# Kernel optimization log

Hardware: AMD Instinct MI355X
Metric: run time of the kernel (lower is better)

The kernel has to match this reference:

```python
import jax, jax.numpy as jnp
import numpy as np

N_QUBITS = 4
N_LAYERS = 6
BATCH = 1 << 20


def _apply_batched_1q(state, U, q):
    # state: [B, 2,2,2,2]; U: [B, 2, 2] per-sample gate on qubit q
    ax = q + 1
    s = jnp.moveaxis(state, ax, -1)
    s = jnp.einsum('bij,b...j->b...i', U, s)
    return jnp.moveaxis(s, -1, ax)


def _apply_shared_1q(state, U, q):
    # U: [2, 2] shared across the batch
    ax = q + 1
    s = jnp.moveaxis(state, ax, -1)
    s = jnp.einsum('ij,...j->...i', U, s)
    return jnp.moveaxis(s, -1, ax)


def _cnot(state, c, t):
    # flip target axis on the control=1 slice
    ca, ta = c + 1, t + 1
    s0 = jax.lax.index_in_dim(state, 0, ca, keepdims=True)
    s1 = jax.lax.index_in_dim(state, 1, ca, keepdims=True)
    return jnp.concatenate([s0, jnp.flip(s1, axis=ta)], axis=ca)


def _circuit(x, weights):
    n = N_QUBITS
    B = x.shape[0]
    # |0...0> state, batched: [B, 2,2,2,2]
    state = jnp.zeros((B,) + (2,) * n, dtype=jnp.complex64)
    state = state.at[(slice(None),) + (0,) * n].set(1.0)
    # Data-encoding RY(x_q) per sample on each wire
    half = x / 2
    c, s = jnp.cos(half), jnp.sin(half)  # [B, n]
    for q in range(n):
        row0 = jnp.stack([c[:, q], -s[:, q]], axis=-1)
        row1 = jnp.stack([s[:, q], c[:, q]], axis=-1)
        U = jnp.stack([row0, row1], axis=-2).astype(jnp.complex64)  # [B,2,2]
        state = _apply_batched_1q(state, U, q)
    # BasicEntanglerLayers: per layer, RX(w) on each wire then CNOT ring
    for l in range(weights.shape[0]):
        for q in range(n):
            t = weights[l, q] / 2
            ct = (jnp.cos(t) + 0j).astype(jnp.complex64)
            st = (-1j * jnp.sin(t)).astype(jnp.complex64)
            U = jnp.stack([jnp.stack([ct, st]), jnp.stack([st, ct])])  # [2,2]
            state = _apply_shared_1q(state, U, q)
        for q in range(n):
            state = _cnot(state, q, (q + 1) % n)
    # <Z_q> from marginal probabilities
    probs = jnp.real(state * jnp.conj(state))  # [B,2,2,2,2] float32
    z = jnp.array([1.0, -1.0], dtype=jnp.float32)
    outs = []
    for q in range(n):
        reduce_axes = tuple(a for a in range(1, n + 1) if a != q + 1)
        outs.append(jnp.tensordot(probs.sum(axis=reduce_axes), z, axes=([1], [0])))
    return jnp.stack(outs, axis=-1)  # [B, n_qubits]


def setup_inputs():
    key = jax.random.key(0)
    k1, k2 = jax.random.split(key)
    x = jax.random.normal(k1, (BATCH, N_QUBITS), dtype=jnp.float32)
    weights = jax.random.normal(k2, (N_LAYERS, N_QUBITS), dtype=jnp.float32) * 0.01
    return {"x": x, "weights": weights}


def reference(x, weights):
    return _circuit(x, weights)
```

## Files before the change

### kernel.cpp

```cpp
#include <hip/hip_runtime.h>
#include <math.h>

#define N_QUBITS 4
#define N_LAYERS 6
#define NW (N_LAYERS * N_QUBITS)

__global__ __launch_bounds__(256) void qprep_kernel(
    const float* __restrict__ weights, float* __restrict__ Ctab)
{
    __shared__ float Wr[16][16];
    __shared__ float Wi[16][16];
    __shared__ float S[4][16][16];
    __shared__ float wc[NW], ws[NW];
    const int tid = threadIdx.x;
    if (tid < NW) {
        float t = weights[tid] * 0.5f;
        wc[tid] = __cosf(t);
        ws[tid] = __sinf(t);
    }
    __syncthreads();

    if (tid < 16) {
        float re[16], im[16];
#pragma unroll
        for (int k = 0; k < 16; ++k) { re[k] = (k == tid) ? 1.f : 0.f; im[k] = 0.f; }
#pragma unroll 1
        for (int l = 0; l < N_LAYERS; ++l) {
#pragma unroll
            for (int q = 0; q < 4; ++q) {
                const float ct = wc[l * 4 + q], sn = ws[l * 4 + q];
                const int mask = 8 >> q;
#pragma unroll
                for (int idx = 0; idx < 16; ++idx) {
                    if (idx & mask) continue;
                    const int j = idx | mask;
                    float r0 = re[idx], u0 = im[idx], r1 = re[j], u1 = im[j];
                    re[idx] = ct * r0 + sn * u1; im[idx] = ct * u0 - sn * r1;
                    re[j]   = ct * r1 + sn * u0; im[j]   = ct * u1 - sn * r0;
                }
            }
#pragma unroll
            for (int q = 0; q < 4; ++q) {
                const int cm = 8 >> q, tm = 8 >> ((q + 1) & 3);
#pragma unroll
                for (int idx = 0; idx < 16; ++idx) {
                    if ((idx & cm) && !(idx & tm)) {
                        const int j = idx | tm;
                        float t0 = re[idx]; re[idx] = re[j]; re[j] = t0;
                        float t1 = im[idx]; im[idx] = im[j]; im[j] = t1;
                    }
                }
            }
        }
#pragma unroll
        for (int k = 0; k < 16; ++k) { Wr[k][tid] = re[k]; Wi[k][tid] = im[k]; }
    }
    __syncthreads();

    {
        const int i = tid >> 4, j = tid & 15;
        float acc0 = 0.f, acc1 = 0.f, acc2 = 0.f, acc3 = 0.f;
#pragma unroll
        for (int k = 0; k < 16; ++k) {
            const float prod = Wr[k][i] * Wr[k][j] + Wi[k][i] * Wi[k][j];
            acc0 += (k & 8) ? -prod : prod;
            acc1 += (k & 4) ? -prod : prod;
            acc2 += (k & 2) ? -prod : prod;
            acc3 += (k & 1) ? -prod : prod;
        }
        S[0][i][j] = acc0; S[1][i][j] = acc1; S[2][i][j] = acc2; S[3][i][j] = acc3;
    }
    __syncthreads();

    if (tid < 81) {
        const int t1 = tid / 27, t2 = (tid / 9) % 3, t3 = (tid / 3) % 3, t4 = tid % 3;
        int zm = 0, xm = 0;
        if (t1 == 1) zm |= 8; else if (t1 == 2) xm |= 8;
        if (t2 == 1) zm |= 4; else if (t2 == 2) xm |= 4;
        if (t3 == 1) zm |= 2; else if (t3 == 2) xm |= 2;
        if (t4 == 1) zm |= 1; else if (t4 == 2) xm |= 1;
#pragma unroll
        for (int q = 0; q < 4; ++q) {
            float acc = 0.f;
#pragma unroll
            for (int i = 0; i < 16; ++i) {
                const float v = S[q][i][i ^ xm];
                acc += (__popc(i & zm) & 1) ? -v : v;
            }
            Ctab[tid * 4 + q] = acc * 0.0625f;
        }
    }
}

__global__ __launch_bounds__(256, 6) void qeval_kernel(
    const float* __restrict__ x, const float* __restrict__ Ctab,
    float* __restrict__ out, int B)
{
    int b = blockIdx.x * 256 + threadIdx.x;
    b = (b < B) ? b : (B - 1);

    const float4 xv = reinterpret_cast<const float4*>(x)[b];
    const float c0 = __cosf(xv.x), s0 = __sinf(xv.x);
    const float c1 = __cosf(xv.y), s1 = __sinf(xv.y);
    const float c2 = __cosf(xv.z), s2 = __sinf(xv.z);
    const float c3 = __cosf(xv.w), s3 = __sinf(xv.w);

    float u9[9], w9[9];
    u9[0] = 1.f;  u9[1] = c1;      u9[2] = s1;
    u9[3] = c0;   u9[4] = c0 * c1; u9[5] = c0 * s1;
    u9[6] = s0;   u9[7] = s0 * c1; u9[8] = s0 * s1;
    w9[0] = 1.f;  w9[1] = c3;      w9[2] = s3;
    w9[3] = c2;   w9[4] = c2 * c3; w9[5] = c2 * s3;
    w9[6] = s2;   w9[7] = s2 * c3; w9[8] = s2 * s3;

    const float4* __restrict__ C4 = reinterpret_cast<const float4*>(Ctab);

    float4 o = make_float4(0.f, 0.f, 0.f, 0.f);
#pragma unroll
    for (int i = 0; i < 9; ++i) {
        float4 t = make_float4(0.f, 0.f, 0.f, 0.f);
#pragma unroll
        for (int j = 0; j < 9; ++j) {
            const float4 c = C4[i * 9 + j];
            const float w = w9[j];
            t.x = fmaf(c.x, w, t.x);
            t.y = fmaf(c.y, w, t.y);
            t.z = fmaf(c.z, w, t.z);
            t.w = fmaf(c.w, w, t.w);
        }
        const float u = u9[i];
        o.x = fmaf(t.x, u, o.x);
        o.y = fmaf(t.y, u, o.y);
        o.z = fmaf(t.z, u, o.z);
        o.w = fmaf(t.w, u, o.w);
    }

    reinterpret_cast<float4*>(out)[b] = o;
}

extern "C" void kernel_launch(void* const* d_in, const int* in_sizes, int n_in,
                              void* d_out, int out_size, void* d_ws, size_t ws_size,
                              hipStream_t stream) {
    const float* x = (const float*)d_in[0];
    const float* weights = (const float*)d_in[1];
    float* out = (float*)d_out;
    float* Ctab = (float*)d_ws;
    const int B = in_sizes[0] / 4;

    qprep_kernel<<<1, 256, 0, stream>>>(weights, Ctab);

    const int grid = (B + 255) / 256;
    qeval_kernel<<<grid, 256, 0, stream>>>(x, Ctab, out, B);
}
```

Measured before the change: 80.61 us.

## Fuse coefficient prep into eval kernel with persistent blocks and readlane broadcast

Merges the table-building and evaluation kernels into one launch of 512 blocks. Each block recomputes the 81x4 coefficient table in shared memory, keeps it in registers and broadcasts entries via readlane, and then processes eight samples per thread in two interleaved streams. This removes a second launch, the global table round-trip and the per-sample table loads, but repeats the serial prep in every block. The grid is hardcoded, so it covers only up to 2^20 samples.

```diff
diff --git a/kernel.cpp b/kernel.cpp
--- a/kernel.cpp
+++ b/kernel.cpp
@@ -1,18 +1,26 @@
 #include <hip/hip_runtime.h>
 #include <math.h>
 
-#define N_QUBITS 4
 #define N_LAYERS 6
-#define NW (N_LAYERS * N_QUBITS)
+#define NW (N_LAYERS * 4)
 
-__global__ __launch_bounds__(256) void qprep_kernel(
-    const float* __restrict__ weights, float* __restrict__ Ctab)
+typedef float vf4 __attribute__((ext_vector_type(4)));
+
+__device__ __forceinline__ float rdl(float v, int lane) {
+    return __int_as_float(__builtin_amdgcn_readlane(__float_as_int(v), lane));
+}
+
+__global__ __launch_bounds__(256, 2) void qfused_kernel(
+    const float* __restrict__ x, const float* __restrict__ weights,
+    float* __restrict__ out, int B)
 {
-    __shared__ float Wr[16][16];
-    __shared__ float Wi[16][16];
-    __shared__ float S[4][16][16];
+    __shared__ float Wr[16][16], Wi[16][16];
+    __shared__ float S4[4][16][16];
     __shared__ float wc[NW], ws[NW];
+    __shared__ vf4 Cs[81];
+
     const int tid = threadIdx.x;
+
     if (tid < NW) {
         float t = weights[tid] * 0.5f;
         wc[tid] = __cosf(t);
@@ -59,16 +67,16 @@
 
     {
         const int i = tid >> 4, j = tid & 15;
-        float acc0 = 0.f, acc1 = 0.f, acc2 = 0.f, acc3 = 0.f;
+        float a0 = 0.f, a1 = 0.f, a2 = 0.f, a3 = 0.f;
 #pragma unroll
         for (int k = 0; k < 16; ++k) {
-            const float prod = Wr[k][i] * Wr[k][j] + Wi[k][i] * Wi[k][j];
-            acc0 += (k & 8) ? -prod : prod;
-            acc1 += (k & 4) ? -prod : prod;
-            acc2 += (k & 2) ? -prod : prod;
-            acc3 += (k & 1) ? -prod : prod;
+            const float p = Wr[k][i] * Wr[k][j] + Wi[k][i] * Wi[k][j];
+            a0 += (k & 8) ? -p : p;
+            a1 += (k & 4) ? -p : p;
+            a2 += (k & 2) ? -p : p;
+            a3 += (k & 1) ? -p : p;
         }
-        S[0][i][j] = acc0; S[1][i][j] = acc1; S[2][i][j] = acc2; S[3][i][j] = acc3;
+        S4[0][i][j] = a0; S4[1][i][j] = a1; S4[2][i][j] = a2; S4[3][i][j] = a3;
     }
     __syncthreads();
 
@@ -79,63 +87,99 @@
         if (t2 == 1) zm |= 4; else if (t2 == 2) xm |= 4;
         if (t3 == 1) zm |= 2; else if (t3 == 2) xm |= 2;
         if (t4 == 1) zm |= 1; else if (t4 == 2) xm |= 1;
+        vf4 c;
 #pragma unroll
         for (int q = 0; q < 4; ++q) {
             float acc = 0.f;
 #pragma unroll
             for (int i = 0; i < 16; ++i) {
-                const float v = S[q][i][i ^ xm];
+                const float v = S4[q][i][i ^ xm];
                 acc += (__popc(i & zm) & 1) ? -v : v;
             }
-            Ctab[tid * 4 + q] = acc * 0.0625f;
+            c[q] = acc * 0.0625f;
         }
+        Cs[tid] = c;
     }
-}
+    __syncthreads();
 
-__global__ __launch_bounds__(256, 6) void qeval_kernel(
-    const float* __restrict__ x, const float* __restrict__ Ctab,
-    float* __restrict__ out, int B)
-{
-    int b = blockIdx.x * 256 + threadIdx.x;
-    b = (b < B) ? b : (B - 1);
+    const int lane = tid & 63;
+    const vf4 Areg = Cs[lane];
+    const vf4 Breg = Cs[64 + (lane < 17 ? lane : 16)];
 
-    const float4 xv = reinterpret_cast<const float4*>(x)[b];
-    const float c0 = __cosf(xv.x), s0 = __sinf(xv.x);
-    const float c1 = __cosf(xv.y), s1 = __sinf(xv.y);
-    const float c2 = __cosf(xv.z), s2 = __sinf(xv.z);
-    const float c3 = __cosf(xv.w), s3 = __sinf(xv.w);
+    const float4* __restrict__ xv4 = reinterpret_cast<const float4*>(x);
+    float4* __restrict__ ov4 = reinterpret_cast<float4*>(out);
+    const int tbase = blockIdx.x * 256 + tid;
+    const int HALF = 512 * 256;
+    const int STRIDE = 2 * HALF;
 
-    float u9[9], w9[9];
-    u9[0] = 1.f;  u9[1] = c1;      u9[2] = s1;
-    u9[3] = c0;   u9[4] = c0 * c1; u9[5] = c0 * s1;
-    u9[6] = s0;   u9[7] = s0 * c1; u9[8] = s0 * s1;
-    w9[0] = 1.f;  w9[1] = c3;      w9[2] = s3;
-    w9[3] = c2;   w9[4] = c2 * c3; w9[5] = c2 * s3;
-    w9[6] = s2;   w9[7] = s2 * c3; w9[8] = s2 * s3;
+#pragma unroll 1
+    for (int k = 0; k < 4; ++k) {
+        int b0 = tbase + k * STRIDE;
+        int b1 = b0 + HALF;
+        b0 = (b0 < B) ? b0 : (B - 1);
+        b1 = (b1 < B) ? b1 : (B - 1);
+        const float4 x0 = xv4[b0];
+        const float4 x1 = xv4[b1];
 
-    const float4* __restrict__ C4 = reinterpret_cast<const float4*>(Ctab);
+        float u9a[9], w9a[9], u9b[9], w9b[9];
+        {
+            const float c0 = __cosf(x0.x), s0 = __sinf(x0.x);
+            const float c1 = __cosf(x0.y), s1 = __sinf(x0.y);
+            const float c2 = __cosf(x0.z), s2 = __sinf(x0.z);
+            const float c3 = __cosf(x0.w), s3 = __sinf(x0.w);
+            u9a[0] = 1.f; u9a[1] = c1;      u9a[2] = s1;
+            u9a[3] = c0;  u9a[4] = c0 * c1; u9a[5] = c0 * s1;
+            u9a[6] = s0;  u9a[7] = s0 * c1; u9a[8] = s0 * s1;
+            w9a[0] = 1.f; w9a[1] = c3;      w9a[2] = s3;
+            w9a[3] = c2;  w9a[4] = c2 * c3; w9a[5] = c2 * s3;
+            w9a[6] = s2;  w9a[7] = s2 * c3; w9a[8] = s2 * s3;
+        }
+        {
+            const float c0 = __cosf(x1.x), s0 = __sinf(x1.x);
+            const float c1 = __cosf(x1.y), s1 = __sinf(x1.y);
+            const float c2 = __cosf(x1.z), s2 = __sinf(x1.z);
+            const float c3 = __cosf(x1.w), s3 = __sinf(x1.w);
+            u9b[0] = 1.f; u9b[1] = c1;      u9b[2] = s1;
+            u9b[3] = c0;  u9b[4] = c0 * c1; u9b[5] = c0 * s1;
+            u9b[6] = s0;  u9b[7] = s0 * c1; u9b[8] = s0 * s1;
+            w9b[0] = 1.f; w9b[1] = c3;      w9b[2] = s3;
+            w9b[3] = c2;  w9b[4] = c2 * c3; w9b[5] = c2 * s3;
+            w9b[6] = s2;  w9b[7] = s2 * c3; w9b[8] = s2 * s3;
+        }
 
-    float4 o = make_float4(0.f, 0.f, 0.f, 0.f);
+        float4 oa = make_float4(0.f, 0.f, 0.f, 0.f);
+        float4 ob = make_float4(0.f, 0.f, 0.f, 0.f);
 #pragma unroll
-    for (int i = 0; i < 9; ++i) {
-        float4 t = make_float4(0.f, 0.f, 0.f, 0.f);
+        for (int i = 0; i < 9; ++i) {
+            float4 ta = make_float4(0.f, 0.f, 0.f, 0.f);
+            float4 tb = make_float4(0.f, 0.f, 0.f, 0.f);
 #pragma unroll
-        for (int j = 0; j < 9; ++j) {
-            const float4 c = C4[i * 9 + j];
-            const float w = w9[j];
-            t.x = fmaf(c.x, w, t.x);
-            t.y = fmaf(c.y, w, t.y);
-            t.z = fmaf(c.z, w, t.z);
-            t.w = fmaf(c.w, w, t.w);
+            for (int j = 0; j < 9; ++j) {
+                const int t = i * 9 + j;
+                float cx, cy, cz, cw;
+                if (t < 64) {
+                    cx = rdl(Areg.x, t); cy = rdl(Areg.y, t);
+                    cz = rdl(Areg.z, t); cw = rdl(Areg.w, t);
+                } else {
+                    cx = rdl(Breg.x, t - 64); cy = rdl(Breg.y, t - 64);
+                    cz = rdl(Breg.z, t - 64); cw = rdl(Breg.w, t - 64);
+                }
+                const float wa = w9a[j], wb = w9b[j];
+                ta.x = fmaf(cx, wa, ta.x); ta.y = fmaf(cy, wa, ta.y);
+                ta.z = fmaf(cz, wa, ta.z); ta.w = fmaf(cw, wa, ta.w);
+                tb.x = fmaf(cx, wb, tb.x); tb.y = fmaf(cy, wb, tb.y);
+                tb.z = fmaf(cz, wb, tb.z); tb.w = fmaf(cw, wb, tb.w);
+            }
+            const float ua = u9a[i], ub = u9b[i];
+            oa.x = fmaf(ta.x, ua, oa.x); oa.y = fmaf(ta.y, ua, oa.y);
+            oa.z = fmaf(ta.z, ua, oa.z); oa.w = fmaf(ta.w, ua, oa.w);
+            ob.x = fmaf(tb.x, ub, ob.x); ob.y = fmaf(tb.y, ub, ob.y);
+            ob.z = fmaf(tb.z, ub, ob.z); ob.w = fmaf(tb.w, ub, ob.w);
         }
-        const float u = u9[i];
-        o.x = fmaf(t.x, u, o.x);
-        o.y = fmaf(t.y, u, o.y);
-        o.z = fmaf(t.z, u, o.z);
-        o.w = fmaf(t.w, u, o.w);
+
+        ov4[b0] = oa;
+        ov4[b1] = ob;
     }
-
-    reinterpret_cast<float4*>(out)[b] = o;
 }
 
 extern "C" void kernel_launch(void* const* d_in, const int* in_sizes, int n_in,
@@ -144,11 +188,7 @@
     const float* x = (const float*)d_in[0];
     const float* weights = (const float*)d_in[1];
     float* out = (float*)d_out;
-    float* Ctab = (float*)d_ws;
     const int B = in_sizes[0] / 4;
 
-    qprep_kernel<<<1, 256, 0, stream>>>(weights, Ctab);
-
-    const int grid = (B + 255) / 256;
-    qeval_kernel<<<grid, 256, 0, stream>>>(x, Ctab, out, B);
+    qfused_kernel<<<512, 256, 0, stream>>>(x, weights, out, B);
 }
```

Measured after the change: 85.24 us. +5.7%, slower.
